# Performance work log

Measured on AMD Instinct MI355X. Metric: run time of the kernel, lower is better.

The kernel has to match this reference:

```python
import jax, jax.numpy as jnp
import numpy as np

NHEAD = 8
MAX_RADIUS = 16
NEG_INF = float('-inf')


def setup_inputs() -> dict:
    key = jax.random.key(0)
    ks = jax.random.split(key, 6)
    B, T, D = 4, 2048, 512
    s = 1.0 / np.sqrt(D)
    return {
        'x': jax.random.normal(ks[0], (B, T, D), dtype=jnp.float32),
        'radius': jax.random.normal(ks[1], (NHEAD,), dtype=jnp.float32),
        'in_proj_weight': jax.random.normal(ks[2], (3 * D, D), dtype=jnp.float32) * s,
        'in_proj_bias': jax.random.normal(ks[3], (3 * D,), dtype=jnp.float32) * 0.02,
        'out_proj_weight': jax.random.normal(ks[4], (D, D), dtype=jnp.float32) * s,
        'out_proj_bias': jax.random.normal(ks[5], (D,), dtype=jnp.float32) * 0.02,
    }


def reference(x, radius, in_proj_weight, in_proj_bias, out_proj_weight, out_proj_bias):
    B, T, D = x.shape
    H = NHEAD
    hd = D // H
    scale = 1.0 / jnp.sqrt(jnp.asarray(hd, dtype=x.dtype))

    # fused QKV projection: [B,T,3D]
    qkv = x @ in_proj_weight.T + in_proj_bias
    q, k, v = jnp.split(qkv, 3, axis=-1)
    q = q.reshape(B, T, H, hd)
    k = k.reshape(B, T, H, hd)
    v = v.reshape(B, T, H, hd)

    # scores [B,H,T,T]
    scores = jnp.einsum('bqhd,bkhd->bhqk', q, k) * scale

    # per-head learned radius band mask
    r = jnp.clip(jax.nn.sigmoid(radius) * MAX_RADIUS, 1.0)  # [H]
    idx = jnp.arange(T)
    rel = jnp.abs(idx[None, :] - idx[:, None]).astype(x.dtype)  # [T,T]
    band = rel[None, :, :] <= r[:, None, None]  # [H,T,T]
    scores = jnp.where(band[None], scores, NEG_INF)

    attn = jax.nn.softmax(scores, axis=-1)
    out = jnp.einsum('bhqk,bkhd->bqhd', attn, v).reshape(B, T, D)
    return out @ out_proj_weight.T + out_proj_bias
```

## Files before the change

### kernel.cpp

```cpp
#include <hip/hip_runtime.h>
#include <hip/hip_bf16.h>
#include <cstdint>

#define T_LEN 2048
#define B_SZ 4
#define D_MOD 512
#define N_HEAD 8
#define HDIM 64
#define QKV_N 1536
#define M_ROWS 8192

typedef uint32_t u32;
typedef uint16_t u16;
typedef __attribute__((ext_vector_type(8))) __bf16 bf16x8;
typedef __attribute__((ext_vector_type(4))) float f32x4;

__device__ __forceinline__ u16 f2bf(float f) {
    u32 u = __builtin_bit_cast(u32, f);
    u32 r = (u + 0x7FFFu + ((u >> 16) & 1u)) >> 16;
    return (u16)r;
}
__device__ __forceinline__ float bf2f(u16 h) {
    u32 u = ((u32)h) << 16;
    return __builtin_bit_cast(float, u);
}

__global__ void cast_kernel(const float* __restrict__ in, u16* __restrict__ out, int n) {
    int i = (blockIdx.x * blockDim.x + threadIdx.x) * 8;
    if (i >= n) return;
    const float4* p = (const float4*)(in + i);
    float4 a = p[0], b = p[1];
    u32 r0 = (u32)f2bf(a.x) | ((u32)f2bf(a.y) << 16);
    u32 r1 = (u32)f2bf(a.z) | ((u32)f2bf(a.w) << 16);
    u32 r2 = (u32)f2bf(b.x) | ((u32)f2bf(b.y) << 16);
    u32 r3 = (u32)f2bf(b.z) | ((u32)f2bf(b.w) << 16);
    *(uint4*)(out + i) = make_uint4(r0, r1, r2, r3);
}

#define BM 128
#define BN 128
#define BK 32

template <bool OUT_BF16>
__global__ __launch_bounds__(256, 2)
void gemm_bt(const u16* __restrict__ A, const u16* __restrict__ B,
             const float* __restrict__ bias, void* __restrict__ C,
             int M, int N, int K)
{
    __shared__ u16 lda[BM * BK];
    __shared__ u16 ldb[BN * BK];
    const int tid  = threadIdx.x;
    const int wave = tid >> 6;
    const int lane = tid & 63;
    const int bn = blockIdx.x, bm = blockIdx.y;
    const int wm = wave >> 1, wn = wave & 1;

    f32x4 acc[4][4] = {};

    const int srow = lane >> 2;
    const int sg   = (lane & 3) ^ (srow & 3);
    const long a_base = (long)bm * BM;
    const long b_base = (long)bn * BN;

    const int fr = lane & 15;
    const int fq = lane >> 4;
    int a_off[4], b_off[4];
#pragma unroll
    for (int i = 0; i < 4; ++i) {
        int ra = wm * 64 + i * 16 + fr;
        a_off[i] = ra * BK + ((fq ^ (ra & 3)) * 8);
        int rb = wn * 64 + i * 16 + fr;
        b_off[i] = rb * BK + ((fq ^ (rb & 3)) * 8);
    }

    for (int kk = 0; kk < K; kk += BK) {
#pragma unroll
        for (int c = 0; c < 2; ++c) {
            int r = wave * 32 + c * 16 + srow;
            const u16* ga = A + (a_base + r) * (long)K + kk + sg * 8;
            __builtin_amdgcn_global_load_lds(
                (const __attribute__((address_space(1))) void*)ga,
                (__attribute__((address_space(3))) void*)&lda[(wave * 32 + c * 16) * BK],
                16, 0, 0);
            const u16* gb = B + (b_base + r) * (long)K + kk + sg * 8;
            __builtin_amdgcn_global_load_lds(
                (const __attribute__((address_space(1))) void*)gb,
                (__attribute__((address_space(3))) void*)&ldb[(wave * 32 + c * 16) * BK],
                16, 0, 0);
        }
        __syncthreads();
        bf16x8 af[4], bfr[4];
#pragma unroll
        for (int i = 0; i < 4; ++i) af[i]  = *(const bf16x8*)&lda[a_off[i]];
#pragma unroll
        for (int i = 0; i < 4; ++i) bfr[i] = *(const bf16x8*)&ldb[b_off[i]];
#pragma unroll
        for (int mi = 0; mi < 4; ++mi)
#pragma unroll
            for (int ni = 0; ni < 4; ++ni)
                acc[mi][ni] = __builtin_amdgcn_mfma_f32_16x16x32_bf16(
                    af[mi], bfr[ni], acc[mi][ni], 0, 0, 0);
        __syncthreads();
    }

    const long row0 = a_base + wm * 64;
    const long col0 = b_base + wn * 64;
#pragma unroll
    for (int mi = 0; mi < 4; ++mi) {
#pragma unroll
        for (int ni = 0; ni < 4; ++ni) {
            long col = col0 + ni * 16 + fr;
            float bv = bias[col];
            long rowb = row0 + mi * 16 + fq * 4;
#pragma unroll
            for (int rr = 0; rr < 4; ++rr) {
                float v = acc[mi][ni][rr] + bv;
                long idx = (rowb + rr) * (long)N + col;
                if (OUT_BF16) ((u16*)C)[idx] = f2bf(v);
                else          ((float*)C)[idx] = v;
            }
        }
    }
}

#define AQ 64
#define AW 16
#define AROWS 96
#define ASTR 66

__global__ __launch_bounds__(256)
void attn_kernel(const u16* __restrict__ qkv, const float* __restrict__ radius,
                 u16* __restrict__ out)
{
    __shared__ u16 ks[AROWS * ASTR];
    __shared__ u16 vs[AROWS * ASTR];

    const int tid = threadIdx.x;
    const int bid = blockIdx.x;
    const int qc = bid & 31;
    const int h  = (bid >> 5) & 7;
    const int b  = bid >> 8;
    const int q0 = qc * AQ;

    float rad = radius[h];
    float r = 16.0f / (1.0f + __expf(-rad));
    r = fmaxf(r, 1.0f);
    const int w = (int)floorf(r);

    for (int cid = tid; cid < AROWS * 8; cid += 256) {
        int row = cid >> 3;
        int ch  = cid & 7;
        int t = q0 - AW + row;
        t = min(max(t, 0), T_LEN - 1);
        const u16* gk = qkv + ((long)(b * T_LEN + t)) * QKV_N + D_MOD + h * HDIM + ch * 8;
        const u16* gv = gk + D_MOD;
        uint4 kv4 = *(const uint4*)gk;
        uint4 vv4 = *(const uint4*)gv;
        u32* kd = (u32*)&ks[row * ASTR + ch * 8];
        u32* vd = (u32*)&vs[row * ASTR + ch * 8];
        kd[0] = kv4.x; kd[1] = kv4.y; kd[2] = kv4.z; kd[3] = kv4.w;
        vd[0] = vv4.x; vd[1] = vv4.y; vd[2] = vv4.z; vd[3] = vv4.w;
    }

    const int qi = tid >> 2;
    const int g  = tid & 3;
    const int q  = q0 + qi;
    const long qrow = (long)(b * T_LEN + q);

    float qreg[16];
    {
        const u16* gq = qkv + qrow * QKV_N + h * HDIM + g * 16;
        uint4 q1 = *(const uint4*)gq;
        uint4 q2 = *(const uint4*)(gq + 8);
        u32 ww[8] = {q1.x, q1.y, q1.z, q1.w, q2.x, q2.y, q2.z, q2.w};
#pragma unroll
        for (int j = 0; j < 8; ++j) {
            qreg[2 * j]     = bf2f((u16)(ww[j] & 0xffffu)) * 0.125f;
            qreg[2 * j + 1] = bf2f((u16)(ww[j] >> 16))     * 0.125f;
        }
    }
    __syncthreads();

    float m = -1e30f, l = 0.0f;
    float acc[16];
#pragma unroll
    for (int d = 0; d < 16; ++d) acc[d] = 0.0f;

    const int colbase = g * 16;
    for (int rel = -w; rel <= w; ++rel) {
        int j = q + rel;
        if (j < 0 || j >= T_LEN) continue;
        int row = qi + AW + rel;
        const u32* kr = (const u32*)&ks[row * ASTR + colbase];
        float s = 0.0f;
#pragma unroll
        for (int dd = 0; dd < 8; ++dd) {
            u32 wv = kr[dd];
            s += qreg[2 * dd]     * bf2f((u16)(wv & 0xffffu));
            s += qreg[2 * dd + 1] * bf2f((u16)(wv >> 16));
        }
        s += __shfl_xor(s, 1);
        s += __shfl_xor(s, 2);
        float mn = fmaxf(m, s);
        float sc = __expf(m - mn);
        float p  = __expf(s - mn);
        m = mn;
        l = l * sc + p;
        const u32* vr = (const u32*)&vs[row * ASTR + colbase];
#pragma unroll
        for (int dd = 0; dd < 8; ++dd) {
            u32 wv = vr[dd];
            acc[2 * dd]     = acc[2 * dd]     * sc + p * bf2f((u16)(wv & 0xffffu));
            acc[2 * dd + 1] = acc[2 * dd + 1] * sc + p * bf2f((u16)(wv >> 16));
        }
    }

    float inv = 1.0f / l;
    u32 o[8];
#pragma unroll
    for (int j2 = 0; j2 < 8; ++j2) {
        u16 lo = f2bf(acc[2 * j2] * inv);
        u16 hi = f2bf(acc[2 * j2 + 1] * inv);
        o[j2] = (u32)lo | ((u32)hi << 16);
    }
    u16* po = out + qrow * D_MOD + h * HDIM + colbase;
    *(uint4*)po       = make_uint4(o[0], o[1], o[2], o[3]);
    *(uint4*)(po + 8) = make_uint4(o[4], o[5], o[6], o[7]);
}

extern "C" void kernel_launch(void* const* d_in, const int* in_sizes, int n_in,
                              void* d_out, int out_size, void* d_ws, size_t ws_size,
                              hipStream_t stream)
{
    (void)in_sizes; (void)n_in; (void)out_size; (void)ws_size;
    const float* x      = (const float*)d_in[0];
    const float* radius = (const float*)d_in[1];
    const float* w_in   = (const float*)d_in[2];
    const float* b_in   = (const float*)d_in[3];
    const float* w_out  = (const float*)d_in[4];
    const float* b_out  = (const float*)d_in[5];
    float* outp = (float*)d_out;

    char* ws = (char*)d_ws;
    u16* x_bf    = (u16*)ws;  ws += (size_t)M_ROWS * D_MOD * 2;
    u16* win_bf  = (u16*)ws;  ws += (size_t)QKV_N * D_MOD * 2;
    u16* wout_bf = (u16*)ws;  ws += (size_t)D_MOD * D_MOD * 2;
    u16* qkv_bf  = (u16*)ws;  ws += (size_t)M_ROWS * QKV_N * 2;
    u16* attn_bf = (u16*)ws;

    cast_kernel<<<(M_ROWS * D_MOD) / 2048, 256, 0, stream>>>(x, x_bf, M_ROWS * D_MOD);
    cast_kernel<<<(QKV_N * D_MOD) / 2048, 256, 0, stream>>>(w_in, win_bf, QKV_N * D_MOD);
    cast_kernel<<<(D_MOD * D_MOD) / 2048, 256, 0, stream>>>(w_out, wout_bf, D_MOD * D_MOD);

    gemm_bt<true ><<<dim3(QKV_N / BN, M_ROWS / BM), 256, 0, stream>>>(
        x_bf, win_bf, b_in, qkv_bf, M_ROWS, QKV_N, D_MOD);
    attn_kernel<<<B_SZ * N_HEAD * (T_LEN / AQ), 256, 0, stream>>>(qkv_bf, radius, attn_bf);
    gemm_bt<false><<<dim3(D_MOD / BN, M_ROWS / BM), 256, 0, stream>>>(
        attn_bf, wout_bf, b_out, outp, M_ROWS, D_MOD, D_MOD);
}
```

Before: 137.9 us.

## Fuse casts, shrink out-proj GEMM tile, process two queries per thread in attention

Merges the three fp32-to-bf16 cast launches into one kernel to cut launch overhead. Makes the GEMM M-tile a template parameter and uses 64-row tiles for the output projection, doubling the block count (from 256 to 512) to better fill the GPU. The attention kernel now handles 128 queries per block, with each thread computing two adjacent queries so each K/V row load and unpack from LDS is shared between them. The LDS row stride changes to avoid bank conflicts. The cost is more registers per thread and fewer attention blocks.

```diff
diff --git a/kernel.cpp b/kernel.cpp
--- a/kernel.cpp
+++ b/kernel.cpp
@@ -25,63 +25,76 @@
     return __builtin_bit_cast(float, u);
 }
 
-__global__ void cast_kernel(const float* __restrict__ in, u16* __restrict__ out, int n) {
-    int i = (blockIdx.x * blockDim.x + threadIdx.x) * 8;
-    if (i >= n) return;
-    const float4* p = (const float4*)(in + i);
-    float4 a = p[0], b = p[1];
-    u32 r0 = (u32)f2bf(a.x) | ((u32)f2bf(a.y) << 16);
-    u32 r1 = (u32)f2bf(a.z) | ((u32)f2bf(a.w) << 16);
-    u32 r2 = (u32)f2bf(b.x) | ((u32)f2bf(b.y) << 16);
-    u32 r3 = (u32)f2bf(b.z) | ((u32)f2bf(b.w) << 16);
-    *(uint4*)(out + i) = make_uint4(r0, r1, r2, r3);
-}
-
-#define BM 128
-#define BN 128
+__global__ void cast3_kernel(const float* __restrict__ a, int na,
+                             const float* __restrict__ b, int nb,
+                             const float* __restrict__ c,
+                             u16* __restrict__ oa, u16* __restrict__ ob, u16* __restrict__ oc) {
+    int i8 = (blockIdx.x * blockDim.x + threadIdx.x) * 8;
+    const float* src; u16* dst; int off;
+    if (i8 < na)           { src = a; dst = oa; off = i8; }
+    else if (i8 < na + nb) { src = b; dst = ob; off = i8 - na; }
+    else                   { src = c; dst = oc; off = i8 - na - nb; }
+    const float4* p = (const float4*)(src + off);
+    float4 x = p[0], y = p[1];
+    u32 r0 = (u32)f2bf(x.x) | ((u32)f2bf(x.y) << 16);
+    u32 r1 = (u32)f2bf(x.z) | ((u32)f2bf(x.w) << 16);
+    u32 r2 = (u32)f2bf(y.x) | ((u32)f2bf(y.y) << 16);
+    u32 r3 = (u32)f2bf(y.z) | ((u32)f2bf(y.w) << 16);
+    *(uint4*)(dst + off) = make_uint4(r0, r1, r2, r3);
+}
+
 #define BK 32
 
-template <bool OUT_BF16>
+template <bool OUT_BF16, int BMt>
 __global__ __launch_bounds__(256, 2)
 void gemm_bt(const u16* __restrict__ A, const u16* __restrict__ B,
              const float* __restrict__ bias, void* __restrict__ C,
              int M, int N, int K)
 {
-    __shared__ u16 lda[BM * BK];
-    __shared__ u16 ldb[BN * BK];
+    constexpr int WM = BMt / 2;
+    constexpr int MI = WM / 16;
+    __shared__ u16 lda[BMt * BK];
+    __shared__ u16 ldb[128 * BK];
     const int tid  = threadIdx.x;
     const int wave = tid >> 6;
     const int lane = tid & 63;
     const int bn = blockIdx.x, bm = blockIdx.y;
     const int wm = wave >> 1, wn = wave & 1;
 
-    f32x4 acc[4][4] = {};
+    f32x4 acc[MI][4] = {};
 
     const int srow = lane >> 2;
     const int sg   = (lane & 3) ^ (srow & 3);
-    const long a_base = (long)bm * BM;
-    const long b_base = (long)bn * BN;
+    const long a_base = (long)bm * BMt;
+    const long b_base = (long)bn * 128;
 
     const int fr = lane & 15;
     const int fq = lane >> 4;
-    int a_off[4], b_off[4];
+    int a_off[MI], b_off[4];
+#pragma unroll
+    for (int i = 0; i < MI; ++i) {
+        int ra = wm * WM + i * 16 + fr;
+        a_off[i] = ra * BK + ((fq ^ (ra & 3)) * 8);
+    }
 #pragma unroll
     for (int i = 0; i < 4; ++i) {
-        int ra = wm * 64 + i * 16 + fr;
-        a_off[i] = ra * BK + ((fq ^ (ra & 3)) * 8);
         int rb = wn * 64 + i * 16 + fr;
         b_off[i] = rb * BK + ((fq ^ (rb & 3)) * 8);
     }
 
     for (int kk = 0; kk < K; kk += BK) {
 #pragma unroll
-        for (int c = 0; c < 2; ++c) {
-            int r = wave * 32 + c * 16 + srow;
+        for (int c = 0; c < BMt / 64; ++c) {
+            int r = wave * (BMt / 4) + c * 16 + srow;
             const u16* ga = A + (a_base + r) * (long)K + kk + sg * 8;
             __builtin_amdgcn_global_load_lds(
                 (const __attribute__((address_space(1))) void*)ga,
-                (__attribute__((address_space(3))) void*)&lda[(wave * 32 + c * 16) * BK],
+                (__attribute__((address_space(3))) void*)&lda[(wave * (BMt / 4) + c * 16) * BK],
                 16, 0, 0);
+        }
+#pragma unroll
+        for (int c = 0; c < 2; ++c) {
+            int r = wave * 32 + c * 16 + srow;
             const u16* gb = B + (b_base + r) * (long)K + kk + sg * 8;
             __builtin_amdgcn_global_load_lds(
                 (const __attribute__((address_space(1))) void*)gb,
@@ -89,13 +102,13 @@
                 16, 0, 0);
         }
         __syncthreads();
-        bf16x8 af[4], bfr[4];
-#pragma unroll
-        for (int i = 0; i < 4; ++i) af[i]  = *(const bf16x8*)&lda[a_off[i]];
+        bf16x8 af[MI], bfr[4];
+#pragma unroll
+        for (int i = 0; i < MI; ++i) af[i]  = *(const bf16x8*)&lda[a_off[i]];
 #pragma unroll
         for (int i = 0; i < 4; ++i) bfr[i] = *(const bf16x8*)&ldb[b_off[i]];
 #pragma unroll
-        for (int mi = 0; mi < 4; ++mi)
+        for (int mi = 0; mi < MI; ++mi)
 #pragma unroll
             for (int ni = 0; ni < 4; ++ni)
                 acc[mi][ni] = __builtin_amdgcn_mfma_f32_16x16x32_bf16(
@@ -103,10 +116,10 @@
         __syncthreads();
     }
 
-    const long row0 = a_base + wm * 64;
+    const long row0 = a_base + wm * WM;
     const long col0 = b_base + wn * 64;
 #pragma unroll
-    for (int mi = 0; mi < 4; ++mi) {
+    for (int mi = 0; mi < MI; ++mi) {
 #pragma unroll
         for (int ni = 0; ni < 4; ++ni) {
             long col = col0 + ni * 16 + fr;
@@ -123,10 +136,19 @@
     }
 }
 
-#define AQ 64
+#define AQ 128
 #define AW 16
-#define AROWS 96
-#define ASTR 66
+#define AROWS (AQ + 2 * AW)
+#define ASTR 70
+
+__device__ __forceinline__ void unpack16(const u32* __restrict__ src, float* __restrict__ dst) {
+#pragma unroll
+    for (int dd = 0; dd < 8; ++dd) {
+        u32 wv = src[dd];
+        dst[2 * dd]     = bf2f((u16)(wv & 0xffffu));
+        dst[2 * dd + 1] = bf2f((u16)(wv >> 16));
+    }
+}
 
 __global__ __launch_bounds__(256)
 void attn_kernel(const u16* __restrict__ qkv, const float* __restrict__ radius,
@@ -137,9 +159,9 @@
 
     const int tid = threadIdx.x;
     const int bid = blockIdx.x;
-    const int qc = bid & 31;
-    const int h  = (bid >> 5) & 7;
-    const int b  = bid >> 8;
+    const int qc = bid & 15;
+    const int h  = (bid >> 4) & 7;
+    const int b  = bid >> 7;
     const int q0 = qc * AQ;
 
     float rad = radius[h];
@@ -147,85 +169,98 @@
     r = fmaxf(r, 1.0f);
     const int w = (int)floorf(r);
 
-    for (int cid = tid; cid < AROWS * 8; cid += 256) {
-        int row = cid >> 3;
-        int ch  = cid & 7;
-        int t = q0 - AW + row;
-        t = min(max(t, 0), T_LEN - 1);
-        const u16* gk = qkv + ((long)(b * T_LEN + t)) * QKV_N + D_MOD + h * HDIM + ch * 8;
+    for (int cid = tid; cid < AROWS * 4; cid += 256) {
+        int row = cid >> 2;
+        int ch  = cid & 3;
+        int t = min(max(q0 - AW + row, 0), T_LEN - 1);
+        const u16* gk = qkv + ((long)(b * T_LEN + t)) * QKV_N + D_MOD + h * HDIM + ch * 16;
         const u16* gv = gk + D_MOD;
-        uint4 kv4 = *(const uint4*)gk;
-        uint4 vv4 = *(const uint4*)gv;
-        u32* kd = (u32*)&ks[row * ASTR + ch * 8];
-        u32* vd = (u32*)&vs[row * ASTR + ch * 8];
-        kd[0] = kv4.x; kd[1] = kv4.y; kd[2] = kv4.z; kd[3] = kv4.w;
-        vd[0] = vv4.x; vd[1] = vv4.y; vd[2] = vv4.z; vd[3] = vv4.w;
-    }
-
-    const int qi = tid >> 2;
-    const int g  = tid & 3;
-    const int q  = q0 + qi;
-    const long qrow = (long)(b * T_LEN + q);
-
-    float qreg[16];
+        uint4 k0 = *(const uint4*)gk, k1 = *(const uint4*)(gk + 8);
+        uint4 v0 = *(const uint4*)gv, v1 = *(const uint4*)(gv + 8);
+        u32* kd = (u32*)&ks[row * ASTR + ch * 18];
+        u32* vd = (u32*)&vs[row * ASTR + ch * 18];
+        kd[0] = k0.x; kd[1] = k0.y; kd[2] = k0.z; kd[3] = k0.w;
+        kd[4] = k1.x; kd[5] = k1.y; kd[6] = k1.z; kd[7] = k1.w;
+        vd[0] = v0.x; vd[1] = v0.y; vd[2] = v0.z; vd[3] = v0.w;
+        vd[4] = v1.x; vd[5] = v1.y; vd[6] = v1.z; vd[7] = v1.w;
+    }
+
+    const int p = tid >> 2;
+    const int g = tid & 3;
+    const int qA = q0 + 2 * p;
+    const int qB = qA + 1;
+    const long rowA = (long)(b * T_LEN + qA);
+    const long rowB = rowA + 1;
+
+    float qregA[16], qregB[16];
     {
-        const u16* gq = qkv + qrow * QKV_N + h * HDIM + g * 16;
-        uint4 q1 = *(const uint4*)gq;
-        uint4 q2 = *(const uint4*)(gq + 8);
-        u32 ww[8] = {q1.x, q1.y, q1.z, q1.w, q2.x, q2.y, q2.z, q2.w};
+        const u16* gq = qkv + rowA * QKV_N + h * HDIM + g * 16;
+        u32 wa[8], wb[8];
+        uint4 t0 = *(const uint4*)gq,              t1 = *(const uint4*)(gq + 8);
+        uint4 t2 = *(const uint4*)(gq + QKV_N),    t3 = *(const uint4*)(gq + QKV_N + 8);
+        wa[0]=t0.x; wa[1]=t0.y; wa[2]=t0.z; wa[3]=t0.w; wa[4]=t1.x; wa[5]=t1.y; wa[6]=t1.z; wa[7]=t1.w;
+        wb[0]=t2.x; wb[1]=t2.y; wb[2]=t2.z; wb[3]=t2.w; wb[4]=t3.x; wb[5]=t3.y; wb[6]=t3.z; wb[7]=t3.w;
 #pragma unroll
         for (int j = 0; j < 8; ++j) {
-            qreg[2 * j]     = bf2f((u16)(ww[j] & 0xffffu)) * 0.125f;
-            qreg[2 * j + 1] = bf2f((u16)(ww[j] >> 16))     * 0.125f;
+            qregA[2 * j]     = bf2f((u16)(wa[j] & 0xffffu)) * 0.125f;
+            qregA[2 * j + 1] = bf2f((u16)(wa[j] >> 16))     * 0.125f;
+            qregB[2 * j]     = bf2f((u16)(wb[j] & 0xffffu)) * 0.125f;
+            qregB[2 * j + 1] = bf2f((u16)(wb[j] >> 16))     * 0.125f;
         }
     }
     __syncthreads();
 
-    float m = -1e30f, l = 0.0f;
-    float acc[16];
-#pragma unroll
-    for (int d = 0; d < 16; ++d) acc[d] = 0.0f;
-
-    const int colbase = g * 16;
-    for (int rel = -w; rel <= w; ++rel) {
-        int j = q + rel;
-        if (j < 0 || j >= T_LEN) continue;
-        int row = qi + AW + rel;
-        const u32* kr = (const u32*)&ks[row * ASTR + colbase];
-        float s = 0.0f;
-#pragma unroll
-        for (int dd = 0; dd < 8; ++dd) {
-            u32 wv = kr[dd];
-            s += qreg[2 * dd]     * bf2f((u16)(wv & 0xffffu));
-            s += qreg[2 * dd + 1] * bf2f((u16)(wv >> 16));
-        }
-        s += __shfl_xor(s, 1);
-        s += __shfl_xor(s, 2);
-        float mn = fmaxf(m, s);
-        float sc = __expf(m - mn);
-        float p  = __expf(s - mn);
-        m = mn;
-        l = l * sc + p;
-        const u32* vr = (const u32*)&vs[row * ASTR + colbase];
-#pragma unroll
-        for (int dd = 0; dd < 8; ++dd) {
-            u32 wv = vr[dd];
-            acc[2 * dd]     = acc[2 * dd]     * sc + p * bf2f((u16)(wv & 0xffffu));
-            acc[2 * dd + 1] = acc[2 * dd + 1] * sc + p * bf2f((u16)(wv >> 16));
-        }
-    }
-
-    float inv = 1.0f / l;
-    u32 o[8];
+    float mA = -1e30f, lA = 0.0f, mB = -1e30f, lB = 0.0f;
+    float accA[16], accB[16];
+#pragma unroll
+    for (int d = 0; d < 16; ++d) { accA[d] = 0.0f; accB[d] = 0.0f; }
+
+    const int imax = 2 * w + 1;
+    for (int i = 0; i <= imax; ++i) {
+        int jrow = 2 * p - w + i;
+        int j = q0 + jrow;
+        int row = jrow + AW;
+        float kf[16];
+        unpack16((const u32*)&ks[row * ASTR + g * 18], kf);
+        float sA = 0.0f, sB = 0.0f;
+#pragma unroll
+        for (int d = 0; d < 16; ++d) { sA += qregA[d] * kf[d]; sB += qregB[d] * kf[d]; }
+        sA += __shfl_xor(sA, 1); sA += __shfl_xor(sA, 2);
+        sB += __shfl_xor(sB, 1); sB += __shfl_xor(sB, 2);
+        bool inb = ((unsigned)j) < (unsigned)T_LEN;
+        bool vA = inb && (i < imax);
+        bool vB = inb && (i > 0);
+        float mnA = fmaxf(mA, vA ? sA : -1e30f);
+        float scA = __expf(mA - mnA);
+        float pA  = vA ? __expf(sA - mnA) : 0.0f;
+        mA = mnA; lA = lA * scA + pA;
+        float mnB = fmaxf(mB, vB ? sB : -1e30f);
+        float scB = __expf(mB - mnB);
+        float pB  = vB ? __expf(sB - mnB) : 0.0f;
+        mB = mnB; lB = lB * scB + pB;
+        float vf[16];
+        unpack16((const u32*)&vs[row * ASTR + g * 18], vf);
+#pragma unroll
+        for (int d = 0; d < 16; ++d) {
+            accA[d] = accA[d] * scA + pA * vf[d];
+            accB[d] = accB[d] * scB + pB * vf[d];
+        }
+    }
+
+    float invA = 1.0f / lA;
+    float invB = 1.0f / lB;
+    u32 oA[8], oB[8];
 #pragma unroll
     for (int j2 = 0; j2 < 8; ++j2) {
-        u16 lo = f2bf(acc[2 * j2] * inv);
-        u16 hi = f2bf(acc[2 * j2 + 1] * inv);
-        o[j2] = (u32)lo | ((u32)hi << 16);
-    }
-    u16* po = out + qrow * D_MOD + h * HDIM + colbase;
-    *(uint4*)po       = make_uint4(o[0], o[1], o[2], o[3]);
-    *(uint4*)(po + 8) = make_uint4(o[4], o[5], o[6], o[7]);
+        oA[j2] = (u32)f2bf(accA[2 * j2] * invA) | ((u32)f2bf(accA[2 * j2 + 1] * invA) << 16);
+        oB[j2] = (u32)f2bf(accB[2 * j2] * invB) | ((u32)f2bf(accB[2 * j2 + 1] * invB) << 16);
+    }
+    u16* poA = out + rowA * D_MOD + h * HDIM + g * 16;
+    u16* poB = out + rowB * D_MOD + h * HDIM + g * 16;
+    *(uint4*)poA       = make_uint4(oA[0], oA[1], oA[2], oA[3]);
+    *(uint4*)(poA + 8) = make_uint4(oA[4], oA[5], oA[6], oA[7]);
+    *(uint4*)poB       = make_uint4(oB[0], oB[1], oB[2], oB[3]);
+    *(uint4*)(poB + 8) = make_uint4(oB[4], oB[5], oB[6], oB[7]);
 }
 
 extern "C" void kernel_launch(void* const* d_in, const int* in_sizes, int n_in,
@@ -248,13 +283,15 @@
     u16* qkv_bf  = (u16*)ws;  ws += (size_t)M_ROWS * QKV_N * 2;
     u16* attn_bf = (u16*)ws;
 
-    cast_kernel<<<(M_ROWS * D_MOD) / 2048, 256, 0, stream>>>(x, x_bf, M_ROWS * D_MOD);
-    cast_kernel<<<(QKV_N * D_MOD) / 2048, 256, 0, stream>>>(w_in, win_bf, QKV_N * D_MOD);
-    cast_kernel<<<(D_MOD * D_MOD) / 2048, 256, 0, stream>>>(w_out, wout_bf, D_MOD * D_MOD);
-
-    gemm_bt<true ><<<dim3(QKV_N / BN, M_ROWS / BM), 256, 0, stream>>>(
+    const int na = M_ROWS * D_MOD;
+    const int nb = QKV_N * D_MOD;
+    const int nc = D_MOD * D_MOD;
+    cast3_kernel<<<(na + nb + nc) / 2048, 256, 0, stream>>>(
+        x, na, w_in, nb, w_out, x_bf, win_bf, wout_bf);
+
+    gemm_bt<true, 128><<<dim3(QKV_N / 128, M_ROWS / 128), 256, 0, stream>>>(
         x_bf, win_bf, b_in, qkv_bf, M_ROWS, QKV_N, D_MOD);
     attn_kernel<<<B_SZ * N_HEAD * (T_LEN / AQ), 256, 0, stream>>>(qkv_bf, radius, attn_bf);
-    gemm_bt<false><<<dim3(D_MOD / BN, M_ROWS / BM), 256, 0, stream>>>(
+    gemm_bt<false, 64><<<dim3(D_MOD / 128, M_ROWS / 64), 256, 0, stream>>>(
         attn_bf, wout_bf, b_out, outp, M_ROWS, D_MOD, D_MOD);
 }
```

Result: faster. 130.4 us (-5.4%).
